# Kernel tuning notes

Measured on AMD Instinct MI355X. Metric: run time of the kernel, lower is better.

Reference implementation:

```python
import jax, jax.numpy as jnp
import numpy as np

# Static hyperparams matching init_kwargs
G, D, N, W, KS, AH, AS = 8, 16, 16, 16, 4, 2, 2


def setup_inputs() -> dict:
    key = jax.random.key(0)
    k1, k2 = jax.random.split(key)
    x = jax.random.normal(k1, (8, 128, 32, 1024), dtype=jnp.float32)
    weight = jax.random.normal(k2, (128, 16, 32, 16), dtype=jnp.float32)
    return {"x": x, "weight": weight}


def reference(x, weight):
    b, c, f, T = x.shape
    # pad time axis by w//2 on both sides, then unfold windows of size W, step KS
    xp = jnp.pad(x, ((0, 0), (0, 0), (0, 0), (W // 2, W // 2)))
    t = (xp.shape[-1] - W) // KS + 1
    tidx = jnp.arange(t)[:, None] * KS + jnp.arange(W)[None, :]  # [t, W]
    xw = xp[..., tidx]                                            # [b, c, f, t, W]
    xw = xw.reshape(b, G, D, f, t, W)
    Wg = weight.reshape(G, N, D, f, W)
    # Fused broadcast-multiply + sum over d and w (the all-ones conv sums d and w)
    s = jnp.einsum('bgdftw,gndfw->btgnf', xw, Wg)                 # [b, t, G, N, f]
    s = s.reshape(b, t, G * N, f)
    # box-sum over frequency with window AH, stride AS (fixed all-ones conv height)
    sp = jnp.pad(s, ((0, 0), (0, 0), (0, 0), (AH // 2, AH // 2)))
    f_out = (sp.shape[-1] - AH) // AS + 1
    fidx = jnp.arange(f_out)[:, None] * AS + jnp.arange(AH)[None, :]  # [f_out, AH]
    y = sp[..., fidx].sum(-1)                                     # [b, t, o, f_out]
    y = jax.nn.leaky_relu(y, 0.01)
    return jnp.transpose(y, (0, 2, 3, 1))                         # [b, o, f_out, t]
```

## Files before the change

### kernel.cpp

```cpp
#include <hip/hip_runtime.h>


typedef __attribute__((ext_vector_type(8))) short short8v;
typedef __attribute__((ext_vector_type(4))) float f32x4;

#define TPB 256

static __device__ __forceinline__ short f2bf(float f) {
    unsigned u = __builtin_bit_cast(unsigned, f);
    u += 0x7FFFu + ((u >> 16) & 1u);
    return (short)(u >> 16);
}

__global__ __launch_bounds__(TPB, 4) void lconv6(
    const float* __restrict__ x,
    const float* __restrict__ wt,
    float* __restrict__ out)
{
    __shared__ __attribute__((aligned(16))) float xl[8320];
    __shared__ float red[4][16];

    const int fo = blockIdx.x, g = blockIdx.y, b = blockIdx.z;
    const int tid  = threadIdx.x;
    const int lane = tid & 63;
    const int wid  = __builtin_amdgcn_readfirstlane(tid >> 6);
    const int cc = lane & 15;
    const int kq = lane >> 4;

    int fvals[2]; int nf = 0;
    if (2*fo - 1 >= 0) fvals[nf++] = 2*fo - 1;
    if (2*fo < 32)     fvals[nf++] = 2*fo;
    const int f0 = fvals[0];
    const int f1 = (nf > 1) ? fvals[1] : f0;

    const int BG = b*128 + g*16;
    const int wlc = (g*16 + cc)*8192 + (kq>>1)*512 + 8*(kq&1);
    const int rbase = (kq>>1)*1040 + 4*cc + 8*(kq&1) + 256*wid;

    auto stage2 = [&](int f_, int dp_, int slot_) {
        #pragma unroll
        for (int r = 0; r < 2; ++r) {
            const float* src = x + ((size_t)((BG + 2*dp_ + r)*32 + f_))*1024 + tid*4;
            __builtin_amdgcn_global_load_lds(
                (const __attribute__((address_space(1))) void*)src,
                (__attribute__((address_space(3))) void*)&xl[slot_*2080 + r*1040 + 8 + tid*4],
                16, 0, 0);
        }
    };

    if (tid < 128) {
        const int row = tid >> 4, p = tid & 15;
        xl[row*1040 + (p < 8 ? p : 1024 + p)] = 0.f;
    }

    stage2(f0, 0, 0);
    stage2(f0, 1, 1);
    stage2(f0, 2, 2);

    f32x4 acc[4];
    #pragma unroll
    for (int t = 0; t < 4; ++t) acc[t] = (f32x4){0.f, 0.f, 0.f, 0.f};

    __syncthreads();

    short8v afr[8];

    for (int s = 0; s < nf; ++s) {
        const int f = (s == 0) ? f0 : f1;

        #pragma unroll
        for (int dp = 0; dp < 8; ++dp) {
            const float* wp = wt + wlc + dp*1024 + f*16;
            const float4 w0 = *(const float4*)wp;
            const float4 w1 = *(const float4*)(wp + 4);
            union { short8v s8; short h[8]; } u;
            u.h[0]=f2bf(w0.x); u.h[1]=f2bf(w0.y); u.h[2]=f2bf(w0.z); u.h[3]=f2bf(w0.w);
            u.h[4]=f2bf(w1.x); u.h[5]=f2bf(w1.y); u.h[6]=f2bf(w1.z); u.h[7]=f2bf(w1.w);
            afr[dp] = u.s8;
        }

        const bool tail = (s == nf - 1);
        #pragma unroll
        for (int dp = 0; dp < 8; ++dp) {
            if (tail && dp == 6)      asm volatile("s_waitcnt vmcnt(2)" ::: "memory");
            else if (tail && dp == 7) asm volatile("s_waitcnt vmcnt(0)" ::: "memory");
            else                      asm volatile("s_waitcnt vmcnt(4)" ::: "memory");
            __builtin_amdgcn_sched_barrier(0);
            __builtin_amdgcn_s_barrier();

            const float* xp = xl + (dp & 3)*2080 + rbase;
            #pragma unroll
            for (int tt = 0; tt < 4; ++tt) {
                const float4 a0 = *(const float4*)(xp + 64*tt);
                const float4 a1 = *(const float4*)(xp + 64*tt + 4);
                union { short8v s8; short h[8]; } ub;
                ub.h[0]=f2bf(a0.x); ub.h[1]=f2bf(a0.y); ub.h[2]=f2bf(a0.z); ub.h[3]=f2bf(a0.w);
                ub.h[4]=f2bf(a1.x); ub.h[5]=f2bf(a1.y); ub.h[6]=f2bf(a1.z); ub.h[7]=f2bf(a1.w);
                acc[tt] = __builtin_amdgcn_mfma_f32_16x16x32_bf16(
                              afr[dp], ub.s8, acc[tt], 0, 0, 0);
            }

            const int q3 = s*8 + dp + 3;
            if (q3 < nf*8) {
                const int f3 = ((q3 >> 3) == 0) ? f0 : f1;
                stage2(f3, (dp + 3) & 7, (dp + 3) & 3);
            }
        }
    }

    __syncthreads();

    {
        float* tp = xl + wid*1088;
        #pragma unroll
        for (int tt = 0; tt < 4; ++tt)
            #pragma unroll
            for (int r = 0; r < 4; ++r) {
                float v = acc[tt][r];
                v = (v > 0.f) ? v : 0.01f*v;
                tp[(kq*4 + r)*68 + tt*16 + cc] = v;
            }
        #pragma unroll
        for (int p = 0; p < 4; ++p) {
            const int linear = p*64 + lane;
            const int nn = linear >> 4;
            const int c4 = linear & 15;
            const float4 vv = *(const float4*)(tp + nn*68 + c4*4);
            const size_t ob = (size_t)(BG + nn)*4369 + (size_t)fo*257
                            + wid*64 + c4*4;
            out[ob + 0] = vv.x; out[ob + 1] = vv.y;
            out[ob + 2] = vv.z; out[ob + 3] = vv.w;
        }
    }

    {
        const int n = tid & 15;
        const int d = tid >> 4;
        const size_t xrow_bg = (size_t)BG * 32768;
        float p = 0.f;
        for (int s = 0; s < nf; ++s) {
            const int f = (s == 0) ? f0 : f1;
            const float* xr = x + xrow_bg + (size_t)d*32768 + (size_t)f*1024 + 1016;
            const float* wr = wt + (size_t)(g*16 + n)*8192 + (size_t)d*512 + f*16;
            #pragma unroll
            for (int w = 0; w < 8; ++w) p = fmaf(xr[w], wr[w], p);
        }
        p += __shfl_xor(p, 16);
        p += __shfl_xor(p, 32);
        if (lane < 16) red[wid][lane] = p;
        __syncthreads();
        if (tid < 16) {
            float v = red[0][tid] + red[1][tid] + red[2][tid] + red[3][tid];
            v = (v > 0.f) ? v : 0.01f*v;
            out[(size_t)(BG + tid)*4369 + (size_t)fo*257 + 256] = v;
        }
    }
}

extern "C" void kernel_launch(void* const* d_in, const int* in_sizes, int n_in,
                              void* d_out, int out_size, void* d_ws, size_t ws_size,
                              hipStream_t stream) {
    const float* x  = (const float*)d_in[0];
    const float* wt = (const float*)d_in[1];
    float* out      = (float*)d_out;
    dim3 grid(17, 8, 8);
    lconv6<<<grid, TPB, 0, stream>>>(x, wt, out);
}
```

Measured before the change: 54.07 us.

## Split time axis across two blocks to double grid and raise occupancy

Each block now covers half of the output time steps, so the grid doubles from 1088 to 2176 blocks, and per-block LDS roughly halves. The padding halo is now filled by redirecting out-of-range loads to a global zero buffer instead of writing zeros into LDS, and launch bounds are raised to 8 blocks per SM. This targets low occupancy and tail imbalance, at the cost of redundant weight loads and bf16 conversions per block plus an extra halo load per stage. The g_zeros buffer relies on device globals being zero-initialised.

```diff
diff --git a/kernel.cpp b/kernel.cpp
--- a/kernel.cpp
+++ b/kernel.cpp
@@ -6,21 +6,24 @@
 
 #define TPB 256
 
+__device__ __attribute__((aligned(64))) float g_zeros[16];
+
 static __device__ __forceinline__ short f2bf(float f) {
     unsigned u = __builtin_bit_cast(unsigned, f);
     u += 0x7FFFu + ((u >> 16) & 1u);
     return (short)(u >> 16);
 }
 
-__global__ __launch_bounds__(TPB, 4) void lconv6(
+__global__ __launch_bounds__(TPB, 8) void lconv8(
     const float* __restrict__ x,
     const float* __restrict__ wt,
     float* __restrict__ out)
 {
-    __shared__ __attribute__((aligned(16))) float xl[8320];
+    __shared__ __attribute__((aligned(16))) float xl[4352];
     __shared__ float red[4][16];
 
-    const int fo = blockIdx.x, g = blockIdx.y, b = blockIdx.z;
+    const int fo = blockIdx.x, g = blockIdx.y;
+    const int b  = blockIdx.z >> 1, th = blockIdx.z & 1;
     const int tid  = threadIdx.x;
     const int lane = tid & 63;
     const int wid  = __builtin_amdgcn_readfirstlane(tid >> 6);
@@ -35,31 +38,45 @@
 
     const int BG = b*128 + g*16;
     const int wlc = (g*16 + cc)*8192 + (kq>>1)*512 + 8*(kq&1);
-    const int rbase = (kq>>1)*1040 + 4*cc + 8*(kq&1) + 256*wid;
+    const int rbase = (kq>>1)*544 + 4*cc + 8*(kq&1) + 128*wid;
 
     auto stage2 = [&](int f_, int dp_, int slot_) {
-        #pragma unroll
-        for (int r = 0; r < 2; ++r) {
-            const float* src = x + ((size_t)((BG + 2*dp_ + r)*32 + f_))*1024 + tid*4;
+        {
+            const int c   = tid;
+            const int r   = (c >= 136) ? 1 : 0;
+            const int c16 = c - r*136;
+            const int tau0 = 4*c16 - 8 + 512*th;
+            const bool ok = (tau0 >= 0) & (tau0 <= 1020);
+            const float* src = ok
+                ? (x + ((size_t)((BG + 2*dp_ + r)*32 + f_))*1024 + tau0)
+                : g_zeros;
             __builtin_amdgcn_global_load_lds(
                 (const __attribute__((address_space(1))) void*)src,
-                (__attribute__((address_space(3))) void*)&xl[slot_*2080 + r*1040 + 8 + tid*4],
+                (__attribute__((address_space(3))) void*)&xl[slot_*1088 + 4*c],
                 16, 0, 0);
         }
+        {
+            const int c16 = 120 + (lane & 15);
+            const int tau0 = 4*c16 - 8 + 512*th;
+            const bool ok = (tau0 >= 0) & (tau0 <= 1020);
+            const float* src = ok
+                ? (x + ((size_t)((BG + 2*dp_ + 1)*32 + f_))*1024 + tau0)
+                : g_zeros;
+            if (lane < 16)
+                __builtin_amdgcn_global_load_lds(
+                    (const __attribute__((address_space(1))) void*)src,
+                    (__attribute__((address_space(3))) void*)&xl[slot_*1088 + 4*(256 + lane)],
+                    16, 0, 0);
+        }
     };
-
-    if (tid < 128) {
-        const int row = tid >> 4, p = tid & 15;
-        xl[row*1040 + (p < 8 ? p : 1024 + p)] = 0.f;
-    }
 
     stage2(f0, 0, 0);
     stage2(f0, 1, 1);
     stage2(f0, 2, 2);
 
-    f32x4 acc[4];
-    #pragma unroll
-    for (int t = 0; t < 4; ++t) acc[t] = (f32x4){0.f, 0.f, 0.f, 0.f};
+    f32x4 acc[2];
+    acc[0] = (f32x4){0.f, 0.f, 0.f, 0.f};
+    acc[1] = (f32x4){0.f, 0.f, 0.f, 0.f};
 
     __syncthreads();
 
@@ -88,9 +105,9 @@
             __builtin_amdgcn_sched_barrier(0);
             __builtin_amdgcn_s_barrier();
 
-            const float* xp = xl + (dp & 3)*2080 + rbase;
+            const float* xp = xl + (dp & 3)*1088 + rbase;
             #pragma unroll
-            for (int tt = 0; tt < 4; ++tt) {
+            for (int tt = 0; tt < 2; ++tt) {
                 const float4 a0 = *(const float4*)(xp + 64*tt);
                 const float4 a1 = *(const float4*)(xp + 64*tt + 4);
                 union { short8v s8; short h[8]; } ub;
@@ -111,29 +128,29 @@
     __syncthreads();
 
     {
-        float* tp = xl + wid*1088;
+        float* tp = xl + wid*576;
         #pragma unroll
-        for (int tt = 0; tt < 4; ++tt)
+        for (int tt = 0; tt < 2; ++tt)
             #pragma unroll
             for (int r = 0; r < 4; ++r) {
                 float v = acc[tt][r];
                 v = (v > 0.f) ? v : 0.01f*v;
-                tp[(kq*4 + r)*68 + tt*16 + cc] = v;
+                tp[(kq*4 + r)*36 + tt*16 + cc] = v;
             }
         #pragma unroll
-        for (int p = 0; p < 4; ++p) {
+        for (int p = 0; p < 2; ++p) {
             const int linear = p*64 + lane;
-            const int nn = linear >> 4;
-            const int c4 = linear & 15;
-            const float4 vv = *(const float4*)(tp + nn*68 + c4*4);
+            const int nn = linear >> 3;
+            const int c4 = linear & 7;
+            const float4 vv = *(const float4*)(tp + nn*36 + c4*4);
             const size_t ob = (size_t)(BG + nn)*4369 + (size_t)fo*257
-                            + wid*64 + c4*4;
+                            + 128*th + 32*wid + 4*c4;
             out[ob + 0] = vv.x; out[ob + 1] = vv.y;
             out[ob + 2] = vv.z; out[ob + 3] = vv.w;
         }
     }
 
-    {
+    if (th == 1) {
         const int n = tid & 15;
         const int d = tid >> 4;
         const size_t xrow_bg = (size_t)BG * 32768;
@@ -163,6 +180,6 @@
     const float* x  = (const float*)d_in[0];
     const float* wt = (const float*)d_in[1];
     float* out      = (float*)d_out;
-    dim3 grid(17, 8, 8);
-    lconv6<<<grid, TPB, 0, stream>>>(x, wt, out);
+    dim3 grid(17, 8, 16);
+    lconv8<<<grid, TPB, 0, stream>>>(x, wt, out);
 }
```

Result: slower. 156.3 us (+189.1%).

## Stage four channel rows per step in a 3-slot ring and prefetch weights

Applied to the files above, without the earlier changes.

Each pipeline stage now loads four d-rows (two d-pairs) instead of two, using a 3-slot LDS ring of larger tiles. Padding zeros come from a global zero buffer instead of explicit LDS zeroing. Weight fragments for the second frequency are loaded into a separate register set during the first frequency's compute. The aim is fewer barriers and waitcnt stalls per unit of MFMA work, at the cost of more LDS (occupancy bound lowered from 4 to 3) and more registers.

```diff
diff --git a/kernel.cpp b/kernel.cpp
--- a/kernel.cpp
+++ b/kernel.cpp
@@ -6,18 +6,20 @@
 
 #define TPB 256
 
+__device__ __attribute__((aligned(64))) float g_zeros[16];
+
 static __device__ __forceinline__ short f2bf(float f) {
     unsigned u = __builtin_bit_cast(unsigned, f);
     u += 0x7FFFu + ((u >> 16) & 1u);
     return (short)(u >> 16);
 }
 
-__global__ __launch_bounds__(TPB, 4) void lconv6(
+__global__ __launch_bounds__(TPB, 3) void lconv12(
     const float* __restrict__ x,
     const float* __restrict__ wt,
     float* __restrict__ out)
 {
-    __shared__ __attribute__((aligned(16))) float xl[8320];
+    __shared__ __attribute__((aligned(16))) float xl[13056];
     __shared__ float red[4][16];
 
     const int fo = blockIdx.x, g = blockIdx.y, b = blockIdx.z;
@@ -30,83 +32,93 @@
     int fvals[2]; int nf = 0;
     if (2*fo - 1 >= 0) fvals[nf++] = 2*fo - 1;
     if (2*fo < 32)     fvals[nf++] = 2*fo;
-    const int f0 = fvals[0];
-    const int f1 = (nf > 1) ? fvals[1] : f0;
 
     const int BG = b*128 + g*16;
     const int wlc = (g*16 + cc)*8192 + (kq>>1)*512 + 8*(kq&1);
-    const int rbase = (kq>>1)*1040 + 4*cc + 8*(kq&1) + 256*wid;
+    const int rbase = (kq>>1)*1088 + 4*cc + 8*(kq&1) + 256*wid;
 
-    auto stage2 = [&](int f_, int dp_, int slot_) {
+    auto stage = [&](int q_) {
+        const int f_ = fvals[q_ >> 2];
+        const int d0 = (q_ & 3) * 4;
+        float* dst = xl + (q_ % 3) * 4352;
+        const float* srcA = x + (size_t)(BG + d0)*32768 + (size_t)f_*1024
+                              + (4*tid - 8);
         #pragma unroll
-        for (int r = 0; r < 2; ++r) {
-            const float* src = x + ((size_t)((BG + 2*dp_ + r)*32 + f_))*1024 + tid*4;
+        for (int k = 0; k < 4; ++k) {
+            const float* src = (tid >= 2) ? (srcA + k*32768) : g_zeros;
             __builtin_amdgcn_global_load_lds(
                 (const __attribute__((address_space(1))) void*)src,
-                (__attribute__((address_space(3))) void*)&xl[slot_*2080 + r*1040 + 8 + tid*4],
+                (__attribute__((address_space(3))) void*)&dst[k*1088 + 4*tid],
                 16, 0, 0);
+        }
+        const int jB  = 256 + (lane & 15);
+        const int tauB = 4*jB - 8;
+        #pragma unroll
+        for (int k = 0; k < 4; ++k) {
+            const float* src = (tauB <= 1020)
+                ? (x + (size_t)(BG + d0 + k)*32768 + (size_t)f_*1024 + tauB)
+                : g_zeros;
+            if (lane < 16)
+                __builtin_amdgcn_global_load_lds(
+                    (const __attribute__((address_space(1))) void*)src,
+                    (__attribute__((address_space(3))) void*)&dst[k*1088 + 4*jB],
+                    16, 0, 0);
         }
     };
 
-    if (tid < 128) {
-        const int row = tid >> 4, p = tid & 15;
-        xl[row*1040 + (p < 8 ? p : 1024 + p)] = 0.f;
-    }
+    auto loadW = [&](short8v (&afr_)[8], int f_) {
+        #pragma unroll
+        for (int dp = 0; dp < 8; ++dp) {
+            const float* wp = wt + wlc + dp*1024 + f_*16;
+            const float4 w0 = *(const float4*)wp;
+            const float4 w1 = *(const float4*)(wp + 4);
+            union { short8v s8; short h[8]; } u;
+            u.h[0]=f2bf(w0.x); u.h[1]=f2bf(w0.y); u.h[2]=f2bf(w0.z); u.h[3]=f2bf(w0.w);
+            u.h[4]=f2bf(w1.x); u.h[5]=f2bf(w1.y); u.h[6]=f2bf(w1.z); u.h[7]=f2bf(w1.w);
+            afr_[dp] = u.s8;
+        }
+    };
 
-    stage2(f0, 0, 0);
-    stage2(f0, 1, 1);
-    stage2(f0, 2, 2);
+    short8v afrA[8], afrB[8];
+    loadW(afrA, fvals[0]);
+    stage(0);
+    stage(1);
 
     f32x4 acc[4];
     #pragma unroll
     for (int t = 0; t < 4; ++t) acc[t] = (f32x4){0.f, 0.f, 0.f, 0.f};
 
-    __syncthreads();
-
-    short8v afr[8];
-
-    for (int s = 0; s < nf; ++s) {
-        const int f = (s == 0) ? f0 : f1;
-
+    auto do_f = [&](const short8v (&afr_)[8], int s) {
         #pragma unroll
-        for (int dp = 0; dp < 8; ++dp) {
-            const float* wp = wt + wlc + dp*1024 + f*16;
-            const float4 w0 = *(const float4*)wp;
-            const float4 w1 = *(const float4*)(wp + 4);
-            union { short8v s8; short h[8]; } u;
-            u.h[0]=f2bf(w0.x); u.h[1]=f2bf(w0.y); u.h[2]=f2bf(w0.z); u.h[3]=f2bf(w0.w);
-            u.h[4]=f2bf(w1.x); u.h[5]=f2bf(w1.y); u.h[6]=f2bf(w1.z); u.h[7]=f2bf(w1.w);
-            afr[dp] = u.s8;
-        }
-
-        const bool tail = (s == nf - 1);
-        #pragma unroll
-        for (int dp = 0; dp < 8; ++dp) {
-            if (tail && dp == 6)      asm volatile("s_waitcnt vmcnt(2)" ::: "memory");
-            else if (tail && dp == 7) asm volatile("s_waitcnt vmcnt(0)" ::: "memory");
-            else                      asm volatile("s_waitcnt vmcnt(4)" ::: "memory");
+        for (int dq = 0; dq < 4; ++dq) {
+            const int q = 4*s + dq;
+            if (q == 4*nf - 1) asm volatile("s_waitcnt vmcnt(0)" ::: "memory");
+            else               asm volatile("s_waitcnt vmcnt(8)" ::: "memory");
             __builtin_amdgcn_sched_barrier(0);
             __builtin_amdgcn_s_barrier();
 
-            const float* xp = xl + (dp & 3)*2080 + rbase;
+            const float* xp = xl + (q % 3)*4352 + rbase;
             #pragma unroll
-            for (int tt = 0; tt < 4; ++tt) {
-                const float4 a0 = *(const float4*)(xp + 64*tt);
-                const float4 a1 = *(const float4*)(xp + 64*tt + 4);
-                union { short8v s8; short h[8]; } ub;
-                ub.h[0]=f2bf(a0.x); ub.h[1]=f2bf(a0.y); ub.h[2]=f2bf(a0.z); ub.h[3]=f2bf(a0.w);
-                ub.h[4]=f2bf(a1.x); ub.h[5]=f2bf(a1.y); ub.h[6]=f2bf(a1.z); ub.h[7]=f2bf(a1.w);
-                acc[tt] = __builtin_amdgcn_mfma_f32_16x16x32_bf16(
-                              afr[dp], ub.s8, acc[tt], 0, 0, 0);
+            for (int jj = 0; jj < 2; ++jj) {
+                const float* xr = xp + jj*2176;
+                #pragma unroll
+                for (int tt = 0; tt < 4; ++tt) {
+                    const float4 a0 = *(const float4*)(xr + 64*tt);
+                    const float4 a1 = *(const float4*)(xr + 64*tt + 4);
+                    union { short8v s8; short h[8]; } ub;
+                    ub.h[0]=f2bf(a0.x); ub.h[1]=f2bf(a0.y); ub.h[2]=f2bf(a0.z); ub.h[3]=f2bf(a0.w);
+                    ub.h[4]=f2bf(a1.x); ub.h[5]=f2bf(a1.y); ub.h[6]=f2bf(a1.z); ub.h[7]=f2bf(a1.w);
+                    acc[tt] = __builtin_amdgcn_mfma_f32_16x16x32_bf16(
+                                  afr_[2*dq + jj], ub.s8, acc[tt], 0, 0, 0);
+                }
             }
+            if (s == 0 && nf == 2 && dq == 3) loadW(afrB, fvals[1]);
+            if (q + 2 <= 4*nf - 1) stage(q + 2);
+        }
+    };
 
-            const int q3 = s*8 + dp + 3;
-            if (q3 < nf*8) {
-                const int f3 = ((q3 >> 3) == 0) ? f0 : f1;
-                stage2(f3, (dp + 3) & 7, (dp + 3) & 3);
-            }
-        }
-    }
+    do_f(afrA, 0);
+    if (nf == 2) do_f(afrB, 1);
 
     __syncthreads();
 
@@ -139,7 +151,7 @@
         const size_t xrow_bg = (size_t)BG * 32768;
         float p = 0.f;
         for (int s = 0; s < nf; ++s) {
-            const int f = (s == 0) ? f0 : f1;
+            const int f = fvals[s];
             const float* xr = x + xrow_bg + (size_t)d*32768 + (size_t)f*1024 + 1016;
             const float* wr = wt + (size_t)(g*16 + n)*8192 + (size_t)d*512 + f*16;
             #pragma unroll
@@ -164,5 +176,5 @@
     const float* wt = (const float*)d_in[1];
     float* out      = (float*)d_out;
     dim3 grid(17, 8, 8);
-    lconv6<<<grid, TPB, 0, stream>>>(x, wt, out);
+    lconv12<<<grid, TPB, 0, stream>>>(x, wt, out);
 }
```

Result: slower. 61.47 us (+13.7%).
